# Performance work log

Hardware: AMD Instinct MI355X
Metric: run time of the kernel (lower is better)

The kernel has to match this reference:

```python
import jax, jax.numpy as jnp
import numpy as np

B, N, D, H, ND = 16, 512, 768, 12, 32
DK = D // H  # 64
GRID = 11    # hard-coded 11x11 patch grid in SpatialCirclePosition.patch


def setup_inputs() -> dict:
    key = jax.random.key(0)
    ks = jax.random.split(key, 10)
    features = jax.random.normal(ks[0], (B, N, D), dtype=jnp.float32)
    boxes = jax.random.uniform(ks[1], (B, N, 4), dtype=jnp.float32)  # normalized [0,1]
    sizes_wh = jax.random.randint(ks[2], (B, 2), 512, 1024).astype(jnp.int32)
    image_sizes = jnp.concatenate([sizes_wh, sizes_wh], axis=-1)  # (B,4) = [w,h,w,h]
    s = 0.02
    Wq = jax.random.normal(ks[3], (D, D), dtype=jnp.float32) * s
    Wk = jax.random.normal(ks[4], (D, D), dtype=jnp.float32) * s
    Wv = jax.random.normal(ks[5], (D, D), dtype=jnp.float32) * s
    Wo = jax.random.normal(ks[6], (D, D), dtype=jnp.float32) * s
    bq = jnp.zeros((D,), jnp.float32); bk = jnp.zeros((D,), jnp.float32)
    bv = jnp.zeros((D,), jnp.float32); bo = jnp.zeros((D,), jnp.float32)
    gamma = jnp.ones((D,), jnp.float32); beta = jnp.zeros((D,), jnp.float32)
    dist_emb = jax.random.normal(ks[7], (ND, H), dtype=jnp.float32) * s
    return {"features": features, "boxes": boxes, "image_sizes": image_sizes,
            "Wq": Wq, "bq": bq, "Wk": Wk, "bk": bk, "Wv": Wv, "bv": bv,
            "Wo": Wo, "bo": bo, "gamma": gamma, "beta": beta, "dist_emb": dist_emb}


def _patch_bins(boxes_norm, image_sizes):
    # boxes_norm: (B,N,4) in [0,1]; image_sizes: (B,4)=[w,h,w,h] int
    sizes_f = image_sizes.astype(jnp.float32)
    boxes = boxes_norm * sizes_f[:, None, :]                       # pixel boxes
    spa = jnp.floor_divide(sizes_f[:, :2], 11.0)                   # (B,2) size_per_area
    lb = jnp.arange(GRID, dtype=jnp.float32)                       # (11,)
    hb = lb + 1.0
    wlb = lb[None, :] * spa[:, 0:1]; whb = hb[None, :] * spa[:, 0:1]   # (B,11)
    hlb = lb[None, :] * spa[:, 1:2]; hhb = hb[None, :] * spa[:, 1:2]
    cx = jnp.floor_divide(boxes[..., 0] + boxes[..., 2], 2.0)      # (B,N)
    cy = jnp.floor_divide(boxes[..., 1] + boxes[..., 3], 2.0)
    mx = (wlb[:, None, :] <= cx[..., None]) & (cx[..., None] <= whb[:, None, :])  # (B,N,11)
    my = (hlb[:, None, :] <= cy[..., None]) & (cy[..., None] <= hhb[:, None, :])
    px = jnp.argmax(mx.astype(jnp.float32), axis=-1)               # (B,N) int
    py = jnp.argmax(my.astype(jnp.float32), axis=-1)
    return px.astype(jnp.float32), py.astype(jnp.float32)


def _dist_bins(boxes_norm, image_sizes):
    px, py = _patch_bins(boxes_norm, image_sizes)
    dx = px[:, None, :] - px[:, :, None]                           # (B,N,N)
    dy = py[:, None, :] - py[:, :, None]
    dist = jnp.sqrt(dx * dx + dy * dy) * 2.0
    return dist.astype(jnp.int32)                                  # truncation == .long()


def reference(features, boxes, image_sizes, Wq, bq, Wk, bk, Wv, bv, Wo, bo, gamma, beta, dist_emb):
    # LayerNorm(d_model), eps matches torch default 1e-5
    mu = jnp.mean(features, axis=-1, keepdims=True)
    var = jnp.mean(jnp.square(features - mu), axis=-1, keepdims=True)
    x = (features - mu) * jax.lax.rsqrt(var + 1e-5) * gamma + beta

    bins = _dist_bins(boxes, image_sizes)                          # (B,N,N) int32
    dist_bias = dist_emb[bins]                                     # (B,N,N,H)
    dist_bias = jnp.transpose(dist_bias, (0, 3, 1, 2))             # (B,H,N,N)

    bsz, nq, _ = x.shape
    q = (x @ Wq.T + bq).reshape(bsz, nq, H, DK).transpose(0, 2, 1, 3)  # (B,H,N,DK)
    k = (x @ Wk.T + bk).reshape(bsz, nq, H, DK).transpose(0, 2, 1, 3)
    v = (x @ Wv.T + bv).reshape(bsz, nq, H, DK).transpose(0, 2, 1, 3)

    att = jnp.einsum('bhqd,bhkd->bhqk', q, k) / np.sqrt(DK).astype(np.float32)
    att = jax.nn.softmax(att + dist_bias, axis=-1)                 # (B,H,N,N)
    out = jnp.einsum('bhqk,bhkd->bhqd', att, v)
    out = out.transpose(0, 2, 1, 3).reshape(bsz, nq, H * DK)
    out = out @ Wo.T + bo
    return out, att
```

## Files before the change

kernel.cpp:

```cpp
#include <hip/hip_runtime.h>
#include <hip/hip_bf16.h>

typedef unsigned char uchar;
typedef __attribute__((ext_vector_type(8))) short bf16x8;
typedef __attribute__((ext_vector_type(4))) float f32x4;

__device__ __forceinline__ unsigned short f2bf(float f) {
  union { float f; unsigned int u; } v; v.f = f;
  unsigned int u = v.u + 0x7fffu + ((v.u >> 16) & 1u);
  return (unsigned short)(u >> 16);
}

__device__ __forceinline__ void async_cp16(void* lds, const void* g) {
  __builtin_amdgcn_global_load_lds(
      (const __attribute__((address_space(1))) unsigned int*)g,
      (__attribute__((address_space(3))) unsigned int*)lds, 16, 0, 0);
}

__global__ void pxpy_kernel(const float* __restrict__ boxes, const int* __restrict__ isz,
                            float* __restrict__ px, float* __restrict__ py) {
  int idx = blockIdx.x * 256 + threadIdx.x;
  int b = idx >> 9;
  float w = (float)isz[b * 4 + 0];
  float h = (float)isz[b * 4 + 1];
  float b0 = boxes[idx * 4 + 0] * w;
  float b1 = boxes[idx * 4 + 1] * h;
  float b2 = boxes[idx * 4 + 2] * w;
  float b3 = boxes[idx * 4 + 3] * h;
  float spw = floorf(w / 11.0f);
  float sph = floorf(h / 11.0f);
  float cx = floorf((b0 + b2) * 0.5f);
  float cy = floorf((b1 + b3) * 0.5f);
  int pxi = 0, pyi = 0;
  bool fx = false, fy = false;
  for (int j = 0; j < 11; ++j) {
    float jf = (float)j;
    if (!fx && jf * spw <= cx && cx <= (jf + 1.0f) * spw) { pxi = j; fx = true; }
    if (!fy && jf * sph <= cy && cy <= (jf + 1.0f) * sph) { pyi = j; fy = true; }
  }
  px[idx] = (float)pxi;
  py[idx] = (float)pyi;
}

__global__ void bins_kernel(const float* __restrict__ px, const float* __restrict__ py,
                            uchar* __restrict__ bins) {
  int r = blockIdx.x;
  int j = threadIdx.x;
  int b = r >> 9;
  float pxq = px[r], pyq = py[r];
  float dx = px[b * 512 + j] - pxq;
  float dy = py[b * 512 + j] - pyq;
  float d = sqrtf(dx * dx + dy * dy) * 2.0f;
  bins[(size_t)r * 512 + j] = (uchar)(int)d;
}

__global__ __launch_bounds__(256) void ln_kernel(const float* __restrict__ f,
                                                 const float* __restrict__ gamma,
                                                 const float* __restrict__ beta,
                                                 unsigned short* __restrict__ x) {
  const int r = blockIdx.x;
  const int t = threadIdx.x;
  const float* row = f + (size_t)r * 768;
  float e0 = row[t], e1 = row[t + 256], e2 = row[t + 512];
  float s = e0 + e1 + e2;
#pragma unroll
  for (int off = 32; off > 0; off >>= 1) s += __shfl_down(s, off);
  __shared__ float red[4];
  const int wid = t >> 6;
  if ((t & 63) == 0) red[wid] = s;
  __syncthreads();
  float mean = (red[0] + red[1] + red[2] + red[3]) * (1.0f / 768.0f);
  __syncthreads();
  float d0 = e0 - mean, d1 = e1 - mean, d2 = e2 - mean;
  float v = d0 * d0 + d1 * d1 + d2 * d2;
#pragma unroll
  for (int off = 32; off > 0; off >>= 1) v += __shfl_down(v, off);
  if ((t & 63) == 0) red[wid] = v;
  __syncthreads();
  float var = (red[0] + red[1] + red[2] + red[3]) * (1.0f / 768.0f);
  float rs = rsqrtf(var + 1e-5f);
  x[(size_t)r * 768 + t]       = f2bf(d0 * rs * gamma[t] + beta[t]);
  x[(size_t)r * 768 + t + 256] = f2bf(d1 * rs * gamma[t + 256] + beta[t + 256]);
  x[(size_t)r * 768 + t + 512] = f2bf(d2 * rs * gamma[t + 512] + beta[t + 512]);
}

__global__ void wprep_kernel(const float* __restrict__ Wq, const float* __restrict__ Wk,
                             const float* __restrict__ Wv, const float* __restrict__ Wo,
                             const float* __restrict__ bq, const float* __restrict__ bk,
                             const float* __restrict__ bv,
                             unsigned short* __restrict__ wcat, unsigned short* __restrict__ wo,
                             float* __restrict__ bcat) {
  int idx = blockIdx.x * 256 + threadIdx.x;
  if (idx < 1769472) {
    int n = idx / 768, k = idx % 768;
    float v = (n < 768) ? Wq[n * 768 + k]
            : (n < 1536) ? Wk[(n - 768) * 768 + k]
                         : Wv[(n - 1536) * 768 + k];
    wcat[idx] = f2bf(v);
  } else {
    int j = idx - 1769472;
    wo[j] = f2bf(Wo[j]);
  }
  if (idx < 2304)
    bcat[idx] = (idx < 768) ? bq[idx] : (idx < 1536) ? bk[idx - 768] : bv[idx - 1536];
}

template <bool OUTF32>
__global__ __launch_bounds__(256) void gemm_bt(const unsigned short* __restrict__ A,
                                               const unsigned short* __restrict__ Bt,
                                               const float* __restrict__ bias,
                                               void* __restrict__ Cout, int K, int ldc) {
  __shared__ unsigned short a_lds[128 * 32];
  __shared__ unsigned short b_lds[128 * 32];
  const int m0 = blockIdx.x * 128, n0 = blockIdx.y * 128;
  const int tid = threadIdx.x;
  const int lane = tid & 63, wid = tid >> 6;
  const int ln = lane & 15, quad = lane >> 4;
  const int wm = (wid & 1) * 64, wn = (wid >> 1) * 64;
  f32x4 acc[16] = {};
  for (int k0 = 0; k0 < K; k0 += 32) {
    __syncthreads();
#pragma unroll
    for (int rep = 0; rep < 2; ++rep) {
      int c = rep * 256 + tid;
      int row = c >> 2, e0 = (c & 3) << 3;
      async_cp16(&a_lds[c * 8], A + (size_t)(m0 + row) * K + k0 + e0);
      async_cp16(&b_lds[c * 8], Bt + (size_t)(n0 + row) * K + k0 + e0);
    }
    __syncthreads();
    bf16x8 af[4], bfr[4];
#pragma unroll
    for (int i = 0; i < 4; ++i)
      af[i] = *(const bf16x8*)&a_lds[(wm + i * 16 + ln) * 32 + quad * 8];
#pragma unroll
    for (int j = 0; j < 4; ++j)
      bfr[j] = *(const bf16x8*)&b_lds[(wn + j * 16 + ln) * 32 + quad * 8];
#pragma unroll
    for (int i = 0; i < 4; ++i)
#pragma unroll
      for (int j = 0; j < 4; ++j)
        acc[i * 4 + j] = __builtin_amdgcn_mfma_f32_16x16x32_bf16(af[i], bfr[j], acc[i * 4 + j], 0, 0, 0);
  }
#pragma unroll
  for (int i = 0; i < 4; ++i)
#pragma unroll
    for (int j = 0; j < 4; ++j)
#pragma unroll
      for (int r = 0; r < 4; ++r) {
        int rr = m0 + wm + i * 16 + quad * 4 + r;
        int cc = n0 + wn + j * 16 + ln;
        float v = acc[i * 4 + j][r] + bias[cc];
        if (OUTF32) ((float*)Cout)[(size_t)rr * ldc + cc] = v;
        else ((unsigned short*)Cout)[(size_t)rr * ldc + cc] = f2bf(v);
      }
}

__global__ __launch_bounds__(256) void attn_fused(const unsigned short* __restrict__ qkv,
                                                  const uchar* __restrict__ bins,
                                                  const float* __restrict__ dist_emb,
                                                  float* __restrict__ att,
                                                  unsigned short* __restrict__ attnout) {
  const int bidx = blockIdx.x;
  const int qt = bidx & 7;
  const int h = (bidx >> 3) % 12;
  const int b = bidx / 96;
  __shared__ unsigned short qs[64 * 72];
  __shared__ unsigned short ks[2][64 * 72];
  __shared__ float demb[32];
  const int tid = threadIdx.x;
  const int lane = tid & 63, wid = tid >> 6;
  const int ln = lane & 15, quad = lane >> 4;
  if (tid < 32) demb[tid] = dist_emb[tid * 12 + h];

  {
    int i0 = tid >> 3, e0 = (tid & 7) * 8;
    *(uint4*)&qs[i0 * 72 + e0] =
        *(const uint4*)(qkv + (size_t)(b * 512 + qt * 64 + i0) * 2304 + h * 64 + e0);
    *(uint4*)&qs[(i0 + 32) * 72 + e0] =
        *(const uint4*)(qkv + (size_t)(b * 512 + qt * 64 + i0 + 32) * 2304 + h * 64 + e0);
  }
  const int si = tid >> 3, se = (tid & 7) * 8;
  const unsigned short* kbase = qkv + (size_t)(b * 512) * 2304 + 768 + h * 64 + se;
  const unsigned short* vbase = qkv + (size_t)(b * 512) * 2304 + 1536 + h * 64 + se;
  uint4 kr0 = *(const uint4*)(kbase + (size_t)si * 2304);
  uint4 kr1 = *(const uint4*)(kbase + (size_t)(si + 32) * 2304);
  __syncthreads();
  bf16x8 a0 = *(const bf16x8*)&qs[(wid * 16 + ln) * 72 + quad * 8];
  bf16x8 a1 = *(const bf16x8*)&qs[(wid * 16 + ln) * 72 + 32 + quad * 8];
  *(uint4*)&ks[0][si * 72 + se] = kr0;
  *(uint4*)&ks[0][(si + 32) * 72 + se] = kr1;
  __syncthreads();
  f32x4 acc[32] = {};
  for (int kc = 0; kc < 8; ++kc) {
    const unsigned short* cur = ks[kc & 1];
    if (kc < 7) {
      kr0 = *(const uint4*)(kbase + (size_t)((kc + 1) * 64 + si) * 2304);
      kr1 = *(const uint4*)(kbase + (size_t)((kc + 1) * 64 + si + 32) * 2304);
    }
    __builtin_amdgcn_s_setprio(1);
#pragma unroll
    for (int t = 0; t < 4; ++t) {
      bf16x8 b0 = *(const bf16x8*)&cur[(t * 16 + ln) * 72 + quad * 8];
      bf16x8 b1 = *(const bf16x8*)&cur[(t * 16 + ln) * 72 + 32 + quad * 8];
      acc[kc * 4 + t] = __builtin_amdgcn_mfma_f32_16x16x32_bf16(a0, b0, acc[kc * 4 + t], 0, 0, 0);
      acc[kc * 4 + t] = __builtin_amdgcn_mfma_f32_16x16x32_bf16(a1, b1, acc[kc * 4 + t], 0, 0, 0);
    }
    __builtin_amdgcn_s_setprio(0);
    if (kc < 7) {
      unsigned short* nxt = ks[(kc + 1) & 1];
      *(uint4*)&nxt[si * 72 + se] = kr0;
      *(uint4*)&nxt[(si + 32) * 72 + se] = kr1;
      __syncthreads();
    }
  }
  uint4 vr0 = *(const uint4*)(vbase + (size_t)si * 2304);
  uint4 vr1 = *(const uint4*)(vbase + (size_t)(si + 32) * 2304);

  const int brow0 = qt * 64 + wid * 16 + quad * 4;
  const uchar* binb = bins + (size_t)b * 512 * 512;
#pragma unroll
  for (int i = 0; i < 32; ++i) {
    int col = (i >> 2) * 64 + (i & 3) * 16 + ln;
#pragma unroll
    for (int r = 0; r < 4; ++r) {
      int bin = binb[(size_t)(brow0 + r) * 512 + col];
      acc[i][r] = acc[i][r] * 0.125f + demb[bin];
    }
  }
  float inv[4];
#pragma unroll
  for (int r = 0; r < 4; ++r) {
    float m = -1e30f;
#pragma unroll
    for (int i = 0; i < 32; ++i) m = fmaxf(m, acc[i][r]);
    m = fmaxf(m, __shfl_xor(m, 1));
    m = fmaxf(m, __shfl_xor(m, 2));
    m = fmaxf(m, __shfl_xor(m, 4));
    m = fmaxf(m, __shfl_xor(m, 8));
    float s = 0.f;
#pragma unroll
    for (int i = 0; i < 32; ++i) { float p = __expf(acc[i][r] - m); acc[i][r] = p; s += p; }
    s += __shfl_xor(s, 1); s += __shfl_xor(s, 2); s += __shfl_xor(s, 4); s += __shfl_xor(s, 8);
    inv[r] = 1.0f / s;
  }
#pragma unroll
  for (int i = 0; i < 32; ++i)
#pragma unroll
    for (int r = 0; r < 4; ++r) acc[i][r] *= inv[r];

  {
    const unsigned short* xs = (const unsigned short*)&vr0;
#pragma unroll
    for (int j = 0; j < 8; ++j) {
      int d = se + j;
      ks[0][d * 72 + (si ^ (((d >> 3) & 7) << 3))] = xs[j];
    }
    xs = (const unsigned short*)&vr1;
#pragma unroll
    for (int j = 0; j < 8; ++j) {
      int d = se + j;
      ks[0][d * 72 + ((si + 32) ^ (((d >> 3) & 7) << 3))] = xs[j];
    }
  }
  __syncthreads();
  f32x4 acc_o[4] = {};
  float* ob = att + (size_t)((b * 12 + h) * 512) * 512;
  for (int kc = 0; kc < 8; ++kc) {
    const unsigned short* cur = ks[kc & 1];
    if (kc < 7) {
      vr0 = *(const uint4*)(vbase + (size_t)((kc + 1) * 64 + si) * 2304);
      vr1 = *(const uint4*)(vbase + (size_t)((kc + 1) * 64 + si + 32) * 2304);
    }
#pragma unroll
    for (int t = 0; t < 4; ++t)
#pragma unroll
      for (int r = 0; r < 4; ++r) {
        int row = wid * 16 + quad * 4 + r;
        int col = (t * 16 + ln) ^ (((row >> 2) & 7) << 3);
        qs[row * 72 + col] = f2bf(acc[kc * 4 + t][r]);
      }
    __builtin_amdgcn_s_setprio(1);
#pragma unroll
    for (int kk = 0; kk < 2; ++kk) {
      int prow = wid * 16 + ln;
      int pcol = (kk * 32 + quad * 8) ^ (((prow >> 2) & 7) << 3);
      bf16x8 af = *(const bf16x8*)&qs[prow * 72 + pcol];
#pragma unroll
      for (int ct = 0; ct < 4; ++ct) {
        int d = ct * 16 + ln;
        int vcol = (kk * 32 + quad * 8) ^ (((d >> 3) & 7) << 3);
        bf16x8 bg = *(const bf16x8*)&cur[d * 72 + vcol];
        acc_o[ct] = __builtin_amdgcn_mfma_f32_16x16x32_bf16(af, bg, acc_o[ct], 0, 0, 0);
      }
    }
    __builtin_amdgcn_s_setprio(0);
#pragma unroll
    for (int t = 0; t < 4; ++t)
#pragma unroll
      for (int r = 0; r < 4; ++r)
        ob[(size_t)(brow0 + r) * 512 + kc * 64 + t * 16 + ln] = acc[kc * 4 + t][r];
    if (kc < 7) {
      unsigned short* nxt = ks[(kc + 1) & 1];
      const unsigned short* xs = (const unsigned short*)&vr0;
#pragma unroll
      for (int j = 0; j < 8; ++j) {
        int d = se + j;
        nxt[d * 72 + (si ^ (((d >> 3) & 7) << 3))] = xs[j];
      }
      xs = (const unsigned short*)&vr1;
#pragma unroll
      for (int j = 0; j < 8; ++j) {
        int d = se + j;
        nxt[d * 72 + ((si + 32) ^ (((d >> 3) & 7) << 3))] = xs[j];
      }
      __syncthreads();
    }
  }
#pragma unroll
  for (int ct = 0; ct < 4; ++ct)
#pragma unroll
    for (int r = 0; r < 4; ++r) {
      int m = b * 512 + qt * 64 + wid * 16 + quad * 4 + r;
      int cc = h * 64 + ct * 16 + ln;
      attnout[(size_t)m * 768 + cc] = f2bf(acc_o[ct][r]);
    }
}

extern "C" void kernel_launch(void* const* d_in, const int* in_sizes, int n_in,
                              void* d_out, int out_size, void* d_ws, size_t ws_size,
                              hipStream_t stream) {
  const float* features = (const float*)d_in[0];
  const float* boxes    = (const float*)d_in[1];
  const int*   isz      = (const int*)d_in[2];
  const float* Wq = (const float*)d_in[3];
  const float* bq = (const float*)d_in[4];
  const float* Wk = (const float*)d_in[5];
  const float* bk = (const float*)d_in[6];
  const float* Wv = (const float*)d_in[7];
  const float* bv = (const float*)d_in[8];
  const float* Wo = (const float*)d_in[9];
  const float* bo = (const float*)d_in[10];
  const float* gamma = (const float*)d_in[11];
  const float* beta  = (const float*)d_in[12];
  const float* dist_emb = (const float*)d_in[13];

  float* out = (float*)d_out;
  float* att = out + (size_t)8192 * 768;

  char* w = (char*)d_ws;
  float* px = (float*)w;          w += 8192 * 4;
  float* py = (float*)w;          w += 8192 * 4;
  uchar* bins = (uchar*)w;        w += (size_t)16 * 512 * 512;
  unsigned short* x = (unsigned short*)w;       w += (size_t)8192 * 768 * 2;
  unsigned short* wcat = (unsigned short*)w;    w += (size_t)2304 * 768 * 2;
  unsigned short* wo = (unsigned short*)w;      w += (size_t)768 * 768 * 2;
  float* bcat = (float*)w;                      w += 2304 * 4;
  unsigned short* qkv = (unsigned short*)w;     w += (size_t)8192 * 2304 * 2;
  unsigned short* attnout = (unsigned short*)w; w += (size_t)8192 * 768 * 2;

  pxpy_kernel<<<32, 256, 0, stream>>>(boxes, isz, px, py);
  bins_kernel<<<8192, 512, 0, stream>>>(px, py, bins);
  ln_kernel<<<8192, 256, 0, stream>>>(features, gamma, beta, x);
  wprep_kernel<<<9216, 256, 0, stream>>>(Wq, Wk, Wv, Wo, bq, bk, bv, wcat, wo, bcat);
  gemm_bt<false><<<dim3(64, 18), 256, 0, stream>>>(x, wcat, bcat, qkv, 768, 2304);
  attn_fused<<<1536, 256, 0, stream>>>(qkv, bins, dist_emb, att, attnout);
  gemm_bt<true><<<dim3(64, 6), 256, 0, stream>>>(attnout, wo, bo, out, 768, 768);
}
```

Measured before the change: 442.2 us.

## Double-buffer GEMM LDS loads, permute bins layout, pack V transpose stores

The GEMM now double-buffers its A/B tiles in LDS, issuing async loads for the next K-slice while MFMAs run on the current one. This removes one barrier per iteration and hides global load latency. The bins tensor is written in a permuted order so the attention kernel can fetch four bins per 32-bit load instead of four byte loads. The V tile transpose now pairs adjacent rows and writes them as one 32-bit LDS store, halving the number of scattered LDS writes. The cost is twice the GEMM LDS footprint and a bins layout that only the attention kernel can read.

```diff
diff --git a/kernel.cpp b/kernel.cpp
--- a/kernel.cpp
+++ b/kernel.cpp
@@ -51,7 +51,8 @@
   float dx = px[b * 512 + j] - pxq;
   float dy = py[b * 512 + j] - pyq;
   float d = sqrtf(dx * dx + dy * dy) * 2.0f;
-  bins[(size_t)r * 512 + j] = (uchar)(int)d;
+  int off = (j >> 6) * 64 + (j & 15) * 4 + ((j >> 4) & 3);
+  bins[(size_t)r * 512 + off] = (uchar)(int)d;
 }
 
 __global__ __launch_bounds__(256) void ln_kernel(const float* __restrict__ f,
@@ -110,37 +111,53 @@
                                                const unsigned short* __restrict__ Bt,
                                                const float* __restrict__ bias,
                                                void* __restrict__ Cout, int K, int ldc) {
-  __shared__ unsigned short a_lds[128 * 32];
-  __shared__ unsigned short b_lds[128 * 32];
+  __shared__ unsigned short a_lds[2][128 * 32];
+  __shared__ unsigned short b_lds[2][128 * 32];
   const int m0 = blockIdx.x * 128, n0 = blockIdx.y * 128;
   const int tid = threadIdx.x;
   const int lane = tid & 63, wid = tid >> 6;
   const int ln = lane & 15, quad = lane >> 4;
   const int wm = (wid & 1) * 64, wn = (wid >> 1) * 64;
+  const int srow = tid >> 2, se0 = (tid & 3) << 3;
   f32x4 acc[16] = {};
-  for (int k0 = 0; k0 < K; k0 += 32) {
-    __syncthreads();
-#pragma unroll
-    for (int rep = 0; rep < 2; ++rep) {
-      int c = rep * 256 + tid;
-      int row = c >> 2, e0 = (c & 3) << 3;
-      async_cp16(&a_lds[c * 8], A + (size_t)(m0 + row) * K + k0 + e0);
-      async_cp16(&b_lds[c * 8], Bt + (size_t)(n0 + row) * K + k0 + e0);
-    }
-    __syncthreads();
+  const int nk = K >> 5;
+#pragma unroll
+  for (int rep = 0; rep < 2; ++rep) {
+    int c = rep * 256 + tid;
+    int row = c >> 2, e0 = (c & 3) << 3;
+    async_cp16(&a_lds[0][c * 8], A + (size_t)(m0 + row) * K + e0);
+    async_cp16(&b_lds[0][c * 8], Bt + (size_t)(n0 + row) * K + e0);
+  }
+  __syncthreads();
+  for (int kc = 0; kc < nk; ++kc) {
+    const int cur = kc & 1;
+    if (kc + 1 < nk) {
+      const int k0 = (kc + 1) << 5;
+#pragma unroll
+      for (int rep = 0; rep < 2; ++rep) {
+        int c = rep * 256 + tid;
+        int row = c >> 2, e0 = (c & 3) << 3;
+        async_cp16(&a_lds[cur ^ 1][c * 8], A + (size_t)(m0 + row) * K + k0 + e0);
+        async_cp16(&b_lds[cur ^ 1][c * 8], Bt + (size_t)(n0 + row) * K + k0 + e0);
+      }
+    }
     bf16x8 af[4], bfr[4];
 #pragma unroll
     for (int i = 0; i < 4; ++i)
-      af[i] = *(const bf16x8*)&a_lds[(wm + i * 16 + ln) * 32 + quad * 8];
+      af[i] = *(const bf16x8*)&a_lds[cur][(wm + i * 16 + ln) * 32 + quad * 8];
 #pragma unroll
     for (int j = 0; j < 4; ++j)
-      bfr[j] = *(const bf16x8*)&b_lds[(wn + j * 16 + ln) * 32 + quad * 8];
+      bfr[j] = *(const bf16x8*)&b_lds[cur][(wn + j * 16 + ln) * 32 + quad * 8];
+    __builtin_amdgcn_s_setprio(1);
 #pragma unroll
     for (int i = 0; i < 4; ++i)
 #pragma unroll
       for (int j = 0; j < 4; ++j)
         acc[i * 4 + j] = __builtin_amdgcn_mfma_f32_16x16x32_bf16(af[i], bfr[j], acc[i * 4 + j], 0, 0, 0);
-  }
+    __builtin_amdgcn_s_setprio(0);
+    __syncthreads();
+  }
+  (void)srow; (void)se0;
 #pragma unroll
   for (int i = 0; i < 4; ++i)
 #pragma unroll
@@ -213,20 +230,22 @@
       __syncthreads();
     }
   }
-  uint4 vr0 = *(const uint4*)(vbase + (size_t)si * 2304);
-  uint4 vr1 = *(const uint4*)(vbase + (size_t)(si + 32) * 2304);
+  uint4 vr0 = *(const uint4*)(vbase + (size_t)(2 * si) * 2304);
+  uint4 vr1 = *(const uint4*)(vbase + (size_t)(2 * si + 1) * 2304);
 
   const int brow0 = qt * 64 + wid * 16 + quad * 4;
   const uchar* binb = bins + (size_t)b * 512 * 512;
 #pragma unroll
-  for (int i = 0; i < 32; ++i) {
-    int col = (i >> 2) * 64 + (i & 3) * 16 + ln;
+  for (int kc8 = 0; kc8 < 8; ++kc8)
 #pragma unroll
     for (int r = 0; r < 4; ++r) {
-      int bin = binb[(size_t)(brow0 + r) * 512 + col];
-      acc[i][r] = acc[i][r] * 0.125f + demb[bin];
-    }
-  }
+      unsigned int b4 = *(const unsigned int*)&binb[(size_t)(brow0 + r) * 512 + kc8 * 64 + ln * 4];
+#pragma unroll
+      for (int t = 0; t < 4; ++t) {
+        int bin = (b4 >> (8 * t)) & 255;
+        acc[kc8 * 4 + t][r] = acc[kc8 * 4 + t][r] * 0.125f + demb[bin];
+      }
+    }
   float inv[4];
 #pragma unroll
   for (int r = 0; r < 4; ++r) {
@@ -249,17 +268,14 @@
     for (int r = 0; r < 4; ++r) acc[i][r] *= inv[r];
 
   {
-    const unsigned short* xs = (const unsigned short*)&vr0;
+    const unsigned short* x0 = (const unsigned short*)&vr0;
+    const unsigned short* x1 = (const unsigned short*)&vr1;
 #pragma unroll
     for (int j = 0; j < 8; ++j) {
       int d = se + j;
-      ks[0][d * 72 + (si ^ (((d >> 3) & 7) << 3))] = xs[j];
-    }
-    xs = (const unsigned short*)&vr1;
-#pragma unroll
-    for (int j = 0; j < 8; ++j) {
-      int d = se + j;
-      ks[0][d * 72 + ((si + 32) ^ (((d >> 3) & 7) << 3))] = xs[j];
+      int col = (2 * si) ^ (((d >> 3) & 7) << 3);
+      unsigned int pk = (unsigned int)x0[j] | ((unsigned int)x1[j] << 16);
+      *(unsigned int*)&ks[0][d * 72 + col] = pk;
     }
   }
   __syncthreads();
@@ -268,8 +284,8 @@
   for (int kc = 0; kc < 8; ++kc) {
     const unsigned short* cur = ks[kc & 1];
     if (kc < 7) {
-      vr0 = *(const uint4*)(vbase + (size_t)((kc + 1) * 64 + si) * 2304);
-      vr1 = *(const uint4*)(vbase + (size_t)((kc + 1) * 64 + si + 32) * 2304);
+      vr0 = *(const uint4*)(vbase + (size_t)((kc + 1) * 64 + 2 * si) * 2304);
+      vr1 = *(const uint4*)(vbase + (size_t)((kc + 1) * 64 + 2 * si + 1) * 2304);
     }
 #pragma unroll
     for (int t = 0; t < 4; ++t)
@@ -301,17 +317,14 @@
         ob[(size_t)(brow0 + r) * 512 + kc * 64 + t * 16 + ln] = acc[kc * 4 + t][r];
     if (kc < 7) {
       unsigned short* nxt = ks[(kc + 1) & 1];
-      const unsigned short* xs = (const unsigned short*)&vr0;
+      const unsigned short* x0 = (const unsigned short*)&vr0;
+      const unsigned short* x1 = (const unsigned short*)&vr1;
 #pragma unroll
       for (int j = 0; j < 8; ++j) {
         int d = se + j;
-        nxt[d * 72 + (si ^ (((d >> 3) & 7) << 3))] = xs[j];
-      }
-      xs = (const unsigned short*)&vr1;
-#pragma unroll
-      for (int j = 0; j < 8; ++j) {
-        int d = se + j;
-        nxt[d * 72 + ((si + 32) ^ (((d >> 3) & 7) << 3))] = xs[j];
+        int col = (2 * si) ^ (((d >> 3) & 7) << 3);
+        unsigned int pk = (unsigned int)x0[j] | ((unsigned int)x1[j] << 16);
+        *(unsigned int*)&nxt[d * 72 + col] = pk;
       }
       __syncthreads();
     }
```

After: 856.1 us. +93.6%, slower.
